# Performance work log

Hardware: AMD Instinct MI355X
Metric: run time of the kernel (lower is better)

The kernel has to match this reference:

```python
import jax, jax.numpy as jnp
import numpy as np

# MinMaxScaler constants (scaler_X / scaler_fitY), baked in since the original
# reads them from sklearn scaler objects.
F_MIN, F_MAX = 0.0, 1.0          # feature_range for both scalers
X_MIN, X_MAX = 0.0, 500.0        # thickness data range (nm)
Y_MIN, Y_MAX = -2000.0, 2000.0   # stress-thickness data range

D_SETS = 256      # number of datasets (rows of process_c)
SEG_LEN = 65536   # thickness samples per dataset


def stress_equation(params, R, P, T, t):
    """Representative instantaneous-stress law, vectorized over [D, L-1].
    params: [D,4]; R,P,T: [D,1]; t: [D,L-1] film thickness."""
    a, b, c, d = params[:, 0:1], params[:, 1:2], params[:, 2:3], params[:, 3:4]
    return (a * jnp.exp(-t / (jnp.abs(c) + 1e-3))
            + b * jnp.log1p(jnp.abs(t))
            + d * R * P / T)


def setup_inputs() -> dict:
    key = jax.random.key(0)
    k1, k2, k3, k4 = jax.random.split(key, 4)
    x_scaled = jax.random.uniform(k1, (D_SETS * SEG_LEN,), dtype=jnp.float32)
    params = jax.random.normal(k2, (D_SETS, 4), dtype=jnp.float32)
    K0 = jax.random.normal(k3, (D_SETS,), dtype=jnp.float32)
    process_c = jax.random.uniform(k4, (D_SETS, 4), dtype=jnp.float32)
    return {"x_scaled": x_scaled, "params": params, "K0": K0, "process_c": process_c}


def reference(x_scaled, params, K0, process_c):
    D = params.shape[0]
    L = x_scaled.shape[0] // D
    # inverse MinMax transform of thickness, then segment view [D, L]
    t = ((x_scaled - F_MIN) / (F_MAX - F_MIN) * (X_MAX - X_MIN) + X_MIN).reshape(D, L)
    R = process_c[:, 0:1]
    T = process_c[:, 1:2] + 0.1   # keep denominator positive
    P = process_c[:, 2:3]
    # Euler integration: Fit[j+1] = Fit[j] + stress(t[j]) * (t[j+1]-t[j]);  Fit[0] = K0
    dT = t[:, 1:] - t[:, :-1]                                # [D, L-1]
    inc = stress_equation(params, R, P, T, t[:, :-1]) * dT   # [D, L-1]
    fit = K0[:, None] + jnp.concatenate(
        [jnp.zeros((D, 1), dtype=x_scaled.dtype), jnp.cumsum(inc, axis=1)], axis=1)
    # forward MinMax transform of the integrated stress
    out = (fit.reshape(-1) - Y_MIN) / (Y_MAX - Y_MIN) * (F_MAX - F_MIN) + F_MIN
    return out
```

## Files before the change

kernel.cpp:

```cpp
#include <hip/hip_runtime.h>

#define NROWS  256
#define LROW   65536
#define BLOCK  1024
#define VPT    16
#define CHUNK  (BLOCK * VPT)
#define NCHUNK (LROW / CHUNK)


__global__ __launch_bounds__(BLOCK)
void stf_scan(const float* __restrict__ x,
              const float* __restrict__ params,
              const float* __restrict__ k0v,
              const float* __restrict__ procc,
              float* __restrict__ out)
{
    const int d    = blockIdx.x;
    const int tid  = threadIdx.x;
    const int lane = tid & 63;
    const int wid  = tid >> 6;

    const float pa  = params[d * 4 + 0];
    const float pb  = params[d * 4 + 1];
    const float pcc = params[d * 4 + 2];
    const float pd  = params[d * 4 + 3];
    const float R   = procc[d * 4 + 0];
    const float T   = procc[d * 4 + 1] + 0.1f;
    const float P   = procc[d * 4 + 2];
    const float inv_c = 1.0f / (fabsf(pcc) + 0.001f);
    const float cterm = pd * R * P / T;
    const float k0  = k0v[d];

    __shared__ float ws[2][17];

    const float* __restrict__ xrow = x   + (size_t)d * LROW;
    float*       __restrict__ orow = out + (size_t)d * LROW;

    float carry = 0.0f;

    float4 cx0, cx1, cx2, cx3;
    {
        const int s0 = tid * VPT;
        cx0 = *(const float4*)(xrow + s0 + 0);
        cx1 = *(const float4*)(xrow + s0 + 4);
        cx2 = *(const float4*)(xrow + s0 + 8);
        cx3 = *(const float4*)(xrow + s0 + 12);
    }
    float xb = 0.0f;
    if (lane == 63) xb = xrow[tid * VPT + VPT];

    for (int ch = 0; ch < NCHUNK; ++ch) {
        const int s = ch * CHUNK + tid * VPT;

        float4 nx0, nx1, nx2, nx3;
        float nxb = 0.0f;
        const bool havenext = (ch + 1 < NCHUNK);
        if (havenext) {
            const int ns = s + CHUNK;
            nx0 = *(const float4*)(xrow + ns + 0);
            nx1 = *(const float4*)(xrow + ns + 4);
            nx2 = *(const float4*)(xrow + ns + 8);
            nx3 = *(const float4*)(xrow + ns + 12);
            if (lane == 63) {
                const int j16 = ns + VPT;
                if (j16 < LROW) nxb = xrow[j16];
            }
        }

        float xn = __shfl_down(cx0.x, 1);
        if (lane == 63) xn = xb;

        float xv[VPT + 1];
        xv[0]  = cx0.x; xv[1]  = cx0.y; xv[2]  = cx0.z; xv[3]  = cx0.w;
        xv[4]  = cx1.x; xv[5]  = cx1.y; xv[6]  = cx1.z; xv[7]  = cx1.w;
        xv[8]  = cx2.x; xv[9]  = cx2.y; xv[10] = cx2.z; xv[11] = cx2.w;
        xv[12] = cx3.x; xv[13] = cx3.y; xv[14] = cx3.z; xv[15] = cx3.w;
        xv[16] = xn;

        float pref[VPT];
        float run = 0.0f;
        #pragma unroll
        for (int k = 0; k < VPT; ++k) {
            const float t0 = xv[k]     * 500.0f;
            const float t1 = xv[k + 1] * 500.0f;
            const float st = pa * __expf(-t0 * inv_c)
                           + pb * __logf(1.0f + t0)
                           + cterm;
            float inc = st * (t1 - t0);
            if (s + k >= LROW - 1) inc = 0.0f;
            run += inc;
            pref[k] = run;
        }

        float v = run;
        #pragma unroll
        for (int off = 1; off < 64; off <<= 1) {
            const float other = __shfl_up(v, off);
            if (lane >= off) v += other;
        }
        const float waveExcl = v - run;

        const int pbuf = ch & 1;
        if (lane == 63) ws[pbuf][wid] = v;
        __syncthreads();
        if (tid == 0) {
            float acc = 0.0f;
            #pragma unroll
            for (int w = 0; w < 16; ++w) {
                const float t = ws[pbuf][w];
                ws[pbuf][w] = acc;
                acc += t;
            }
            ws[pbuf][16] = acc;
        }
        __syncthreads();

        const float blockExcl = carry + ws[pbuf][wid] + waveExcl;
        const float total     = ws[pbuf][16];

        const float basev = k0 + blockExcl;
        float4 o0, o1, o2, o3;
        o0.x = basev;
        o0.y = basev + pref[0];
        o0.z = basev + pref[1];
        o0.w = basev + pref[2];
        o1.x = basev + pref[3];
        o1.y = basev + pref[4];
        o1.z = basev + pref[5];
        o1.w = basev + pref[6];
        o2.x = basev + pref[7];
        o2.y = basev + pref[8];
        o2.z = basev + pref[9];
        o2.w = basev + pref[10];
        o3.x = basev + pref[11];
        o3.y = basev + pref[12];
        o3.z = basev + pref[13];
        o3.w = basev + pref[14];

        const float sc = 2.5e-4f, of = 0.5f;
        o0.x = o0.x * sc + of; o0.y = o0.y * sc + of; o0.z = o0.z * sc + of; o0.w = o0.w * sc + of;
        o1.x = o1.x * sc + of; o1.y = o1.y * sc + of; o1.z = o1.z * sc + of; o1.w = o1.w * sc + of;
        o2.x = o2.x * sc + of; o2.y = o2.y * sc + of; o2.z = o2.z * sc + of; o2.w = o2.w * sc + of;
        o3.x = o3.x * sc + of; o3.y = o3.y * sc + of; o3.z = o3.z * sc + of; o3.w = o3.w * sc + of;

        *(float4*)(orow + s + 0)  = o0;
        *(float4*)(orow + s + 4)  = o1;
        *(float4*)(orow + s + 8)  = o2;
        *(float4*)(orow + s + 12) = o3;

        carry += total;
        if (havenext) { cx0 = nx0; cx1 = nx1; cx2 = nx2; cx3 = nx3; xb = nxb; }
    }
}

extern "C" void kernel_launch(void* const* d_in, const int* in_sizes, int n_in,
                              void* d_out, int out_size, void* d_ws, size_t ws_size,
                              hipStream_t stream) {
    const float* x      = (const float*)d_in[0];
    const float* params = (const float*)d_in[1];
    const float* K0     = (const float*)d_in[2];
    const float* procc  = (const float*)d_in[3];
    float* out = (float*)d_out;

    stf_scan<<<NROWS, BLOCK, 0, stream>>>(x, params, K0, procc, out);
}
```

Before: 127.8 us.

## Split each row across eight blocks with decoupled lookback carry propagation

Replaces the one-block-per-row sequential chunk loop with 2048 blocks of 512 threads, each handling one 8192-element tile. Blocks publish their tile totals through flag-packed 64-bit atomics in workspace and sum the totals of earlier tiles in the same row to get their carry. The aim is more parallelism and memory-level concurrency than 256 blocks can give. It also switches exp/log to exp2/log2 with folded constants and fuses the output scaling into FMAs. In exchange it adds a memset launch and spin-waiting that relies on earlier blocks being scheduled first.

New measurement: 247.1 us. +93.3%, slower.

```diff
diff --git a/kernel.cpp b/kernel.cpp
--- a/kernel.cpp
+++ b/kernel.cpp
@@ -1,21 +1,26 @@
 #include <hip/hip_runtime.h>
 
-#define NROWS  256
-#define LROW   65536
-#define BLOCK  1024
-#define VPT    16
-#define CHUNK  (BLOCK * VPT)
-#define NCHUNK (LROW / CHUNK)
+#define NROWS 256
+#define LROW  65536
+#define TOT   ((size_t)NROWS * LROW)
+#define BLOCK 512
+#define VPT   16
+#define TILE  (BLOCK * VPT)
+#define TPR   (LROW / TILE)
+#define NTILE (NROWS * TPR)
 
 
 __global__ __launch_bounds__(BLOCK)
-void stf_scan(const float* __restrict__ x,
-              const float* __restrict__ params,
-              const float* __restrict__ k0v,
-              const float* __restrict__ procc,
-              float* __restrict__ out)
+void stf_scan2(const float* __restrict__ x,
+               const float* __restrict__ params,
+               const float* __restrict__ k0v,
+               const float* __restrict__ procc,
+               float* __restrict__ out,
+               unsigned long long* __restrict__ state)
 {
-    const int d    = blockIdx.x;
+    const int bid  = blockIdx.x;
+    const int d    = bid >> 3;
+    const int sub  = bid & 7;
     const int tid  = threadIdx.x;
     const int lane = tid & 63;
     const int wid  = tid >> 6;
@@ -27,130 +32,122 @@
     const float R   = procc[d * 4 + 0];
     const float T   = procc[d * 4 + 1] + 0.1f;
     const float P   = procc[d * 4 + 2];
-    const float inv_c = 1.0f / (fabsf(pcc) + 0.001f);
+    const float ec    = -1.44269504f / (fabsf(pcc) + 0.001f);
+    const float pb2   = pb * 0.69314718f;
     const float cterm = pd * R * P / T;
-    const float k0  = k0v[d];
+    const float k0    = k0v[d];
 
-    __shared__ float ws[2][17];
+    const size_t row0 = (size_t)d * LROW;
+    const int    g0   = sub * TILE + tid * VPT;
+    const float* __restrict__ xp = x + row0 + g0;
 
-    const float* __restrict__ xrow = x   + (size_t)d * LROW;
-    float*       __restrict__ orow = out + (size_t)d * LROW;
+    float4 c0 = *(const float4*)(xp + 0);
+    float4 c1 = *(const float4*)(xp + 4);
+    float4 c2 = *(const float4*)(xp + 8);
+    float4 c3 = *(const float4*)(xp + 12);
+    float xb = 0.0f;
+    if (lane == 63) {
+        const size_t gi = row0 + g0 + VPT;
+        if (gi < TOT) xb = x[gi];
+    }
+    float xn = __shfl_down(c0.x, 1);
+    if (lane == 63) xn = xb;
 
-    float carry = 0.0f;
+    float tv[VPT + 1];
+    tv[0]  = c0.x * 500.0f; tv[1]  = c0.y * 500.0f; tv[2]  = c0.z * 500.0f; tv[3]  = c0.w * 500.0f;
+    tv[4]  = c1.x * 500.0f; tv[5]  = c1.y * 500.0f; tv[6]  = c1.z * 500.0f; tv[7]  = c1.w * 500.0f;
+    tv[8]  = c2.x * 500.0f; tv[9]  = c2.y * 500.0f; tv[10] = c2.z * 500.0f; tv[11] = c2.w * 500.0f;
+    tv[12] = c3.x * 500.0f; tv[13] = c3.y * 500.0f; tv[14] = c3.z * 500.0f; tv[15] = c3.w * 500.0f;
+    tv[16] = xn * 500.0f;
 
-    float4 cx0, cx1, cx2, cx3;
-    {
-        const int s0 = tid * VPT;
-        cx0 = *(const float4*)(xrow + s0 + 0);
-        cx1 = *(const float4*)(xrow + s0 + 4);
-        cx2 = *(const float4*)(xrow + s0 + 8);
-        cx3 = *(const float4*)(xrow + s0 + 12);
+    const bool isLast = (sub == TPR - 1) && (tid == BLOCK - 1);
+
+    float pref[VPT];
+    float run = 0.0f;
+    #pragma unroll
+    for (int k = 0; k < VPT; ++k) {
+        const float t0 = tv[k];
+        const float st = pa * exp2f(t0 * ec) + pb2 * __log2f(1.0f + t0) + cterm;
+        float inc = st * (tv[k + 1] - t0);
+        if (k == VPT - 1) inc = isLast ? 0.0f : inc;
+        run += inc;
+        pref[k] = run;
     }
-    float xb = 0.0f;
-    if (lane == 63) xb = xrow[tid * VPT + VPT];
 
-    for (int ch = 0; ch < NCHUNK; ++ch) {
-        const int s = ch * CHUNK + tid * VPT;
+    float v = run;
+    #pragma unroll
+    for (int off = 1; off < 64; off <<= 1) {
+        const float other = __shfl_up(v, off);
+        if (lane >= off) v += other;
+    }
+    const float waveExcl = v - run;
 
-        float4 nx0, nx1, nx2, nx3;
-        float nxb = 0.0f;
-        const bool havenext = (ch + 1 < NCHUNK);
-        if (havenext) {
-            const int ns = s + CHUNK;
-            nx0 = *(const float4*)(xrow + ns + 0);
-            nx1 = *(const float4*)(xrow + ns + 4);
-            nx2 = *(const float4*)(xrow + ns + 8);
-            nx3 = *(const float4*)(xrow + ns + 12);
-            if (lane == 63) {
-                const int j16 = ns + VPT;
-                if (j16 < LROW) nxb = xrow[j16];
-            }
+    __shared__ float wtot[8];
+    __shared__ float wexcl[8];
+    __shared__ float s_carry;
+    if (lane == 63) wtot[wid] = v;
+    __syncthreads();
+
+    if (wid == 0) {
+        float wv = (lane < 8) ? wtot[lane] : 0.0f;
+        float iv = wv;
+        #pragma unroll
+        for (int off = 1; off < 8; off <<= 1) {
+            const float o = __shfl_up(iv, off);
+            if (lane >= off && lane < 8) iv += o;
+        }
+        if (lane < 8) wexcl[lane] = iv - wv;
+        const float total = __shfl(iv, 7);
+
+        if (lane == 0) {
+            const unsigned long long packed =
+                0x100000000ull | (unsigned long long)__float_as_uint(total);
+            __hip_atomic_store(&state[bid], packed,
+                               __ATOMIC_RELEASE, __HIP_MEMORY_SCOPE_AGENT);
         }
 
-        float xn = __shfl_down(cx0.x, 1);
-        if (lane == 63) xn = xb;
+        float c = 0.0f;
+        if (lane < sub) {
+            const int pt = bid - 1 - lane;
+            unsigned long long w;
+            do {
+                w = __hip_atomic_load(&state[pt],
+                                      __ATOMIC_ACQUIRE, __HIP_MEMORY_SCOPE_AGENT);
+            } while (!(w >> 32));
+            c = __uint_as_float((unsigned)w);
+        }
+        #pragma unroll
+        for (int off = 1; off < 8; off <<= 1) c += __shfl_xor(c, off);
+        if (lane == 0) s_carry = c;
+    }
+    __syncthreads();
 
-        float xv[VPT + 1];
-        xv[0]  = cx0.x; xv[1]  = cx0.y; xv[2]  = cx0.z; xv[3]  = cx0.w;
-        xv[4]  = cx1.x; xv[5]  = cx1.y; xv[6]  = cx1.z; xv[7]  = cx1.w;
-        xv[8]  = cx2.x; xv[9]  = cx2.y; xv[10] = cx2.z; xv[11] = cx2.w;
-        xv[12] = cx3.x; xv[13] = cx3.y; xv[14] = cx3.z; xv[15] = cx3.w;
-        xv[16] = xn;
+    const float sc    = 2.5e-4f;
+    const float obase = (k0 + s_carry + wexcl[wid] + waveExcl) * sc + 0.5f;
 
-        float pref[VPT];
-        float run = 0.0f;
-        #pragma unroll
-        for (int k = 0; k < VPT; ++k) {
-            const float t0 = xv[k]     * 500.0f;
-            const float t1 = xv[k + 1] * 500.0f;
-            const float st = pa * __expf(-t0 * inv_c)
-                           + pb * __logf(1.0f + t0)
-                           + cterm;
-            float inc = st * (t1 - t0);
-            if (s + k >= LROW - 1) inc = 0.0f;
-            run += inc;
-            pref[k] = run;
-        }
+    float4 o0, o1, o2, o3;
+    o0.x = obase;
+    o0.y = fmaf(pref[0],  sc, obase);
+    o0.z = fmaf(pref[1],  sc, obase);
+    o0.w = fmaf(pref[2],  sc, obase);
+    o1.x = fmaf(pref[3],  sc, obase);
+    o1.y = fmaf(pref[4],  sc, obase);
+    o1.z = fmaf(pref[5],  sc, obase);
+    o1.w = fmaf(pref[6],  sc, obase);
+    o2.x = fmaf(pref[7],  sc, obase);
+    o2.y = fmaf(pref[8],  sc, obase);
+    o2.z = fmaf(pref[9],  sc, obase);
+    o2.w = fmaf(pref[10], sc, obase);
+    o3.x = fmaf(pref[11], sc, obase);
+    o3.y = fmaf(pref[12], sc, obase);
+    o3.z = fmaf(pref[13], sc, obase);
+    o3.w = fmaf(pref[14], sc, obase);
 
-        float v = run;
-        #pragma unroll
-        for (int off = 1; off < 64; off <<= 1) {
-            const float other = __shfl_up(v, off);
-            if (lane >= off) v += other;
-        }
-        const float waveExcl = v - run;
-
-        const int pbuf = ch & 1;
-        if (lane == 63) ws[pbuf][wid] = v;
-        __syncthreads();
-        if (tid == 0) {
-            float acc = 0.0f;
-            #pragma unroll
-            for (int w = 0; w < 16; ++w) {
-                const float t = ws[pbuf][w];
-                ws[pbuf][w] = acc;
-                acc += t;
-            }
-            ws[pbuf][16] = acc;
-        }
-        __syncthreads();
-
-        const float blockExcl = carry + ws[pbuf][wid] + waveExcl;
-        const float total     = ws[pbuf][16];
-
-        const float basev = k0 + blockExcl;
-        float4 o0, o1, o2, o3;
-        o0.x = basev;
-        o0.y = basev + pref[0];
-        o0.z = basev + pref[1];
-        o0.w = basev + pref[2];
-        o1.x = basev + pref[3];
-        o1.y = basev + pref[4];
-        o1.z = basev + pref[5];
-        o1.w = basev + pref[6];
-        o2.x = basev + pref[7];
-        o2.y = basev + pref[8];
-        o2.z = basev + pref[9];
-        o2.w = basev + pref[10];
-        o3.x = basev + pref[11];
-        o3.y = basev + pref[12];
-        o3.z = basev + pref[13];
-        o3.w = basev + pref[14];
-
-        const float sc = 2.5e-4f, of = 0.5f;
-        o0.x = o0.x * sc + of; o0.y = o0.y * sc + of; o0.z = o0.z * sc + of; o0.w = o0.w * sc + of;
-        o1.x = o1.x * sc + of; o1.y = o1.y * sc + of; o1.z = o1.z * sc + of; o1.w = o1.w * sc + of;
-        o2.x = o2.x * sc + of; o2.y = o2.y * sc + of; o2.z = o2.z * sc + of; o2.w = o2.w * sc + of;
-        o3.x = o3.x * sc + of; o3.y = o3.y * sc + of; o3.z = o3.z * sc + of; o3.w = o3.w * sc + of;
-
-        *(float4*)(orow + s + 0)  = o0;
-        *(float4*)(orow + s + 4)  = o1;
-        *(float4*)(orow + s + 8)  = o2;
-        *(float4*)(orow + s + 12) = o3;
-
-        carry += total;
-        if (havenext) { cx0 = nx0; cx1 = nx1; cx2 = nx2; cx3 = nx3; xb = nxb; }
-    }
+    float* __restrict__ op = out + row0 + g0;
+    *(float4*)(op + 0)  = o0;
+    *(float4*)(op + 4)  = o1;
+    *(float4*)(op + 8)  = o2;
+    *(float4*)(op + 12) = o3;
 }
 
 extern "C" void kernel_launch(void* const* d_in, const int* in_sizes, int n_in,
@@ -161,6 +158,8 @@
     const float* K0     = (const float*)d_in[2];
     const float* procc  = (const float*)d_in[3];
     float* out = (float*)d_out;
+    unsigned long long* state = (unsigned long long*)d_ws;
 
-    stf_scan<<<NROWS, BLOCK, 0, stream>>>(x, params, K0, procc, out);
+    hipMemsetAsync(d_ws, 0, NTILE * sizeof(unsigned long long), stream);
+    stf_scan2<<<NTILE, BLOCK, 0, stream>>>(x, params, K0, procc, out, state);
 }
```
